# Kernel tuning notes

Measured on AMD Instinct MI355X. Metric: run time of the kernel, lower is better.

## Reference

```python
import jax, jax.numpy as jnp
import numpy as np

B, T, D, R = 8, 4096, 1024, 1024
INIT = 0.02

def setup_inputs() -> dict:
    key = jax.random.key(0)
    ks = jax.random.split(key, 8)
    x = jax.random.normal(ks[0], (B, T, D), dtype=jnp.float32)
    attention_mask = jnp.ones((B, T), dtype=bool)
    W_Q = jax.random.normal(ks[1], (D, D), dtype=jnp.float32) * (1.0 / np.sqrt(D))
    W_K = jax.random.normal(ks[2], (D, D), dtype=jnp.float32) * (1.0 / np.sqrt(D))
    U = jax.random.normal(ks[3], (D, R), dtype=jnp.float32) * INIT
    V = jax.random.normal(ks[4], (D, R), dtype=jnp.float32) * INIT
    Wb = jax.random.normal(ks[5], (D, R), dtype=jnp.float32) * INIT
    bias = jnp.zeros((D,), dtype=jnp.float32)
    W_O = jax.random.normal(ks[6], (D, D), dtype=jnp.float32) * (1.0 / np.sqrt(D))
    return {"x": x, "attention_mask": attention_mask, "W_Q": W_Q, "W_K": W_K,
            "U": U, "V": V, "Wb": Wb, "bias": bias, "W_O": W_O}

def reference(x, attention_mask, W_Q, W_K, U, V, Wb, bias, W_O):
    # Q = x @ W_Q^T, K = x @ W_K^T  (torch Linear stores weight as (out,in))
    Q = jnp.einsum('btd,ed->bte', x, W_Q)
    K = jnp.einsum('btd,ed->bte', x, W_K)
    m = attention_mask.astype(x.dtype)               # (B,T)
    A = Q @ V                                        # (B,T,R)  = Q_i V
    Kw = (K @ Wb) * m[..., None]                     # pad-masked K_j W
    S = jnp.cumsum(Kw, axis=1)                       # causal prefix sum over j<=i
    n = jnp.cumsum(m, axis=1)[..., None]             # n_valid per i, (B,T,1)
    # sum_{j<=i} BCN(Q_i,K_j) = ((Q_iV) * S_i) U^T + n_i * bias; then divide by max(n_i,1)
    out = ((A * S) @ U.T + n * bias) / jnp.clip(n, 1.0)
    return jnp.einsum('btd,ed->bte', out, W_O)
```

## Files before the change

kernel.cpp:

```cpp
#include <hip/hip_runtime.h>
#include <hip/hip_bf16.h>

typedef __attribute__((ext_vector_type(8))) short short8;
typedef __attribute__((ext_vector_type(4))) float f32x4;

#define Bc 8
#define Tc 4096
#define Dc 1024
#define Rc 1024
#define BT (Bc*Tc)

__device__ inline float b2f(ushort u) {
    union { float f; unsigned int i; } x; x.i = ((unsigned int)u) << 16; return x.f;
}
__device__ inline ushort f2b(float f) {
    union { float f; unsigned int i; } x; x.f = f;
    unsigned int r = x.i + 0x7fffu + ((x.i >> 16) & 1u);
    return (ushort)(r >> 16);
}

__device__ inline void gload16(const void* g, void* l) {
    __builtin_amdgcn_global_load_lds(
        (const __attribute__((address_space(1))) unsigned int*)g,
        (__attribute__((address_space(3))) unsigned int*)l, 16, 0, 0);
}


__device__ __attribute__((always_inline)) inline
short8 lds_frag(const char* mat, int rowbase, int k, int fr, int hi) {
    const int row = rowbase + fr;
    const int byte = (row << 7) + (((k << 6) + (hi << 4)) ^ ((row & 7) << 4));
    return *(const short8*)(mat + byte);
}

template<int KK>
__device__ __attribute__((always_inline)) inline
void rdb(const char* BB, short8 (&bf)[2][4], int wn, int fr, int hi) {
#pragma unroll
    for (int n = 0; n < 4; ++n)
        bf[KK][n] = lds_frag(BB, (wn << 6) + (n << 4), KK, fr, hi);
}

template<int MQ, int KK>
__device__ __attribute__((always_inline)) inline
void rda(const char* AB, short8 (&af)[4], int wm, int fr, int hi) {
#pragma unroll
    for (int i = 0; i < 4; ++i)
        af[i] = lds_frag(AB, (wm << 7) + ((MQ * 4 + i) << 4), KK, fr, hi);
}

template<int MQ, int KK>
__device__ __attribute__((always_inline)) inline
void mmq(f32x4 (&acc)[8][4], const short8 (&af)[4], const short8 (&bf)[2][4]) {
#pragma unroll
    for (int i = 0; i < 4; ++i)
#pragma unroll
        for (int n = 0; n < 4; ++n)
            acc[MQ * 4 + i][n] = __builtin_amdgcn_mfma_f32_16x16x32_bf16(
                af[i], bf[KK][n], acc[MQ * 4 + i][n], 0, 0, 0);
}

#define PH_MID do { __builtin_amdgcn_sched_barrier(0); __builtin_amdgcn_s_barrier(); \
    __builtin_amdgcn_s_setprio(1); } while (0)
#define PH_END do { __builtin_amdgcn_s_setprio(0); __builtin_amdgcn_sched_barrier(0); \
    __builtin_amdgcn_s_barrier(); } while (0)

#define STG(G, ld, thr, grow0, gk, lbase) do { \
    const ushort* _p = (G) + (size_t)(grow0) * (ld) + (gk); \
    gload16(_p + (thr), (lbase) + thrD); \
    gload16(_p + (size_t)64 * (ld) + (thr), (lbase) + thrD + 8192); } while (0)

#define TILE(cAb, cBb, stA, stB, tn, tn2) do { \
     \
    rdb<0>(cBb, bf, wn, fr, hi); \
    rda<0, 0>(cAb, afA, wm, fr, hi); \
    rda<1, 0>(cAb, afB, wm, fr, hi); \
    STG(A, lda, thrA, m0, (tn) << 6, stA); \
    PH_MID; mmq<0, 0>(acc, afA, bf); PH_END; \
     \
    rdb<1>(cBb, bf, wn, fr, hi); \
    rda<0, 1>(cAb, afA, wm, fr, hi); \
    STG(A, lda, thrA, m0 + 128, (tn) << 6, stA + 16384); \
    PH_MID; mmq<1, 0>(acc, afB, bf); PH_END; \
     \
    rda<1, 1>(cAb, afB, wm, fr, hi); \
    PH_MID; mmq<0, 1>(acc, afA, bf); PH_END; \
     \
    STG(Bt, ldb, thrB, n0,       (tn2) << 6, stB); \
    STG(Bt, ldb, thrB, n0 + 128, (tn2) << 6, stB + 16384); \
    PH_MID; mmq<1, 1>(acc, afB, bf); \
    __builtin_amdgcn_s_setprio(0); __builtin_amdgcn_sched_barrier(0); \
    asm volatile("s_waitcnt vmcnt(4)" ::: "memory"); \
    __builtin_amdgcn_s_barrier(); } while (0)

template<int EPI>
__global__ __launch_bounds__(512, 2)
void gemm256(const ushort* __restrict__ A, const ushort* __restrict__ Bt,
             void* __restrict__ Cout, const float* __restrict__ bias,
             int ntx, int K, int lda, int ldb, int ldc) {
    __shared__ __align__(16) char sA[65536];
    __shared__ __align__(16) char sB[65536];

    const int tid = threadIdx.x;
    const int w = tid >> 6, l = tid & 63;
    const int wm = w >> 2, wn = w & 3;
    const int fr = l & 15, hi = l >> 4;
    const int srow = (w << 3) + (l >> 3);
    const int scg = (((l & 7) ^ (l >> 3)) << 3);
    const size_t thrA = (size_t)srow * lda + scg;
    const size_t thrB = (size_t)srow * ldb + scg;
    const int thrD = (w << 10) + (l << 4);

    const int nwg = (int)gridDim.x;
    const int q = nwg >> 3;
    const int bid = (int)blockIdx.x;
    const int swz = (bid & 7) * q + (bid >> 3);
    const int by = swz / ntx, bx = swz % ntx;
    const int m0 = by << 8, n0 = bx << 8;

    f32x4 acc[8][4] = {};
    short8 afA[4], afB[4], bf[2][4];
    const int NT = K >> 6;

    STG(A,  lda, thrA, m0,        0,  sA);
    STG(A,  lda, thrA, m0 + 128,  0,  sA + 16384);
    STG(Bt, ldb, thrB, n0,        0,  sB);
    STG(Bt, ldb, thrB, n0 + 128,  0,  sB + 16384);
    STG(Bt, ldb, thrB, n0,        64, sB + 32768);
    STG(Bt, ldb, thrB, n0 + 128,  64, sB + 32768 + 16384);
    asm volatile("s_waitcnt vmcnt(4)" ::: "memory");
    __builtin_amdgcn_sched_barrier(0);
    __builtin_amdgcn_s_barrier();

    const char* cA0 = sA;
    const char* cB0 = sB;
    const char* cA1 = sA + 32768;
    const char* cB1 = sB + 32768;

    for (int it = 0; it < (NT >> 1); ++it) {
        const int t1 = 2 * it + 1;
        const int t2 = min(2 * it + 2, NT - 1);
        const int t3 = min(2 * it + 3, NT - 1);
        TILE(cA0, cB0, sA + 32768, sB, t1, t2);
        TILE(cA1, cB1, sA, sB + 32768, t2, t3);
    }

    const int crow = m0 + (wm << 7);
    const int ccol = n0 + (wn << 6);
#pragma unroll
    for (int m = 0; m < 8; ++m) {
#pragma unroll
        for (int n = 0; n < 4; ++n) {
            const int r0 = crow + (m << 4) + (hi << 2);
            const int c = ccol + (n << 4) + fr;
            if (EPI == 0) {
                ushort* C = (ushort*)Cout;
#pragma unroll
                for (int t = 0; t < 4; ++t)
                    C[(size_t)(r0 + t) * ldc + c] = f2b(acc[m][n][t]);
            } else {
                float* C = (float*)Cout;
                const float bv = bias[c];
#pragma unroll
                for (int t = 0; t < 4; ++t)
                    C[(size_t)(r0 + t) * ldc + c] = acc[m][n][t] + bv;
            }
        }
    }
}

__global__ void cast_f32_bf16(const float4* __restrict__ in, ushort4* __restrict__ out, int n4) {
    int i = blockIdx.x * blockDim.x + threadIdx.x;
    int stride = gridDim.x * blockDim.x;
    for (; i < n4; i += stride) {
        float4 v = in[i];
        ushort4 o;
        o.x = f2b(v.x); o.y = f2b(v.y); o.z = f2b(v.z); o.w = f2b(v.w);
        out[i] = o;
    }
}

__global__ void prep_weights(const float* __restrict__ V,  const float* __restrict__ Wb,
                             const float* __restrict__ U,  const float* __restrict__ WQ,
                             const float* __restrict__ WK, const float* __restrict__ WO,
                             ushort* __restrict__ Vt,  ushort* __restrict__ Wbt,
                             ushort* __restrict__ Ut,  ushort* __restrict__ WQt,
                             ushort* __restrict__ WKt, ushort* __restrict__ WOb) {
    __shared__ float tile[32][33];
    const float* in; ushort* out;
    switch (blockIdx.z) {
        case 0: in = V;  out = Vt;  break;
        case 1: in = Wb; out = Wbt; break;
        case 2: in = U;  out = Ut;  break;
        case 3: in = WQ; out = WQt; break;
        case 4: in = WK; out = WKt; break;
        default: in = WO; out = WOb; break;
    }
    int c0 = blockIdx.x * 32, r0 = blockIdx.y * 32;
    int tx = threadIdx.x & 31, ty = threadIdx.x >> 5;
    if (blockIdx.z < 5) {
        for (int i = 0; i < 32; i += 8)
            tile[ty + i][tx] = in[(size_t)(r0 + ty + i) * 1024 + c0 + tx];
        __syncthreads();
        for (int i = 0; i < 32; i += 8)
            out[(size_t)(c0 + ty + i) * 1024 + r0 + tx] = f2b(tile[tx][ty + i]);
    } else {
        for (int i = 0; i < 32; i += 8)
            out[(size_t)(r0 + ty + i) * 1024 + c0 + tx] =
                f2b(in[(size_t)(r0 + ty + i) * 1024 + c0 + tx]);
    }
}

__global__ __launch_bounds__(256)
void gemm_bt3(const ushort* __restrict__ Vt,  const ushort* __restrict__ WQt,
              const ushort* __restrict__ Wbt, const ushort* __restrict__ WKt,
              const ushort* __restrict__ WOb, const ushort* __restrict__ Ut,
              ushort* __restrict__ W1, ushort* __restrict__ Mmat) {
    const ushort *A, *Bt; ushort* Cout;
    switch (blockIdx.z) {
        case 0: A = Vt;  Bt = WQt; Cout = W1; break;
        case 1: A = Wbt; Bt = WKt; Cout = W1 + (size_t)Rc * Dc; break;
        default: A = WOb; Bt = Ut; Cout = Mmat; break;
    }
    __shared__ __align__(16) ushort As[128][32];
    __shared__ __align__(16) ushort Bs[128][32];
    const int tid = threadIdx.x;
    const int wave = tid >> 6, lane = tid & 63;
    const int m0 = blockIdx.y * 128, n0 = blockIdx.x * 128;
    const int wr = (wave >> 1) * 64, wc = (wave & 1) * 64;

    f32x4 acc[4][4] = {};

    const int rS = wave * 32 + (lane >> 2);
    const int kS = (lane & 3) * 8;
    const int fr = lane & 15;
    const int fq = (lane >> 4) * 8;

    for (int kt = 0; kt < 32; ++kt) {
        const int k0 = kt << 5;
        __syncthreads();
        gload16(A  + (size_t)(m0 + rS) * 1024      + k0 + kS, &As[rS][kS]);
        gload16(A  + (size_t)(m0 + rS + 16) * 1024 + k0 + kS, &As[rS + 16][kS]);
        gload16(Bt + (size_t)(n0 + rS) * 1024      + k0 + kS, &Bs[rS][kS]);
        gload16(Bt + (size_t)(n0 + rS + 16) * 1024 + k0 + kS, &Bs[rS + 16][kS]);
        __syncthreads();

        short8 af[4], bfr[4];
        #pragma unroll
        for (int i = 0; i < 4; i++) af[i]  = *(const short8*)&As[wr + i * 16 + fr][fq];
        #pragma unroll
        for (int i = 0; i < 4; i++) bfr[i] = *(const short8*)&Bs[wc + i * 16 + fr][fq];
        #pragma unroll
        for (int i = 0; i < 4; i++)
            #pragma unroll
            for (int j = 0; j < 4; j++)
                acc[i][j] = __builtin_amdgcn_mfma_f32_16x16x32_bf16(af[i], bfr[j], acc[i][j], 0, 0, 0);
    }

    const int rq = (lane >> 4) * 4;
    #pragma unroll
    for (int i = 0; i < 4; i++) {
        #pragma unroll
        for (int j = 0; j < 4; j++) {
            int row = m0 + wr + i * 16 + rq;
            int col = n0 + wc + j * 16 + fr;
            #pragma unroll
            for (int t = 0; t < 4; t++)
                Cout[(size_t)(row + t) * 1024 + col] = f2b(acc[i][j][t]);
        }
    }
}

__global__ void bias_O_kernel(const float* __restrict__ W_O, const float* __restrict__ bias,
                              float* __restrict__ biasO) {
    __shared__ float sh[256];
    int e = blockIdx.x, tid = threadIdx.x;
    float s = 0.f;
    for (int d = tid; d < Dc; d += 256) s += W_O[(size_t)e * Dc + d] * bias[d];
    sh[tid] = s; __syncthreads();
    for (int o = 128; o > 0; o >>= 1) { if (tid < o) sh[tid] += sh[tid + o]; __syncthreads(); }
    if (tid == 0) biasO[e] = sh[0];
}

__global__ void mask_scan(const int* __restrict__ mask, float* __restrict__ nbuf) {
    __shared__ float sh[256];
    int b = blockIdx.x, tid = threadIdx.x;
    float run = 0.f;
    for (int t0 = 0; t0 < Tc; t0 += 256) {
        float v = (mask[b * Tc + t0 + tid] != 0) ? 1.f : 0.f;
        sh[tid] = v; __syncthreads();
        for (int off = 1; off < 256; off <<= 1) {
            float add = (tid >= off) ? sh[tid - off] : 0.f;
            __syncthreads();
            sh[tid] += add;
            __syncthreads();
        }
        nbuf[b * Tc + t0 + tid] = run + sh[tid];
        run += sh[255];
        __syncthreads();
    }
}

#define NCHUNK 64
#define LCHUNK (Tc / NCHUNK)

__global__ void scan_partial(const ushort* __restrict__ AKw, const int* __restrict__ mask,
                             float* __restrict__ csum) {
    const int r = threadIdx.x * 4;
    const int chunk = blockIdx.x, b = blockIdx.y;
    const int row0 = b * Tc + chunk * LCHUNK;
    const ushort* p = AKw + (size_t)row0 * 2048 + 1024 + r;
    float4 s = {0.f, 0.f, 0.f, 0.f};
    for (int t = 0; t < LCHUNK; ++t) {
        if (mask[row0 + t] != 0) {
            ushort4 q = *(const ushort4*)(p + (size_t)t * 2048);
            s.x += b2f(q.x); s.y += b2f(q.y); s.z += b2f(q.z); s.w += b2f(q.w);
        }
    }
    *(float4*)(csum + (((size_t)b * NCHUNK + chunk) << 10) + r) = s;
}

__global__ void scan_offsets(float* __restrict__ csum) {
    const int r = threadIdx.x * 4;
    const int b = blockIdx.x;
    float4 run = {0.f, 0.f, 0.f, 0.f};
    for (int c = 0; c < NCHUNK; ++c) {
        float4* p = (float4*)(csum + (((size_t)b * NCHUNK + c) << 10) + r);
        float4 v = *p; *p = run;
        run.x += v.x; run.y += v.y; run.z += v.z; run.w += v.w;
    }
}

__global__ void scan_apply(ushort* __restrict__ AKw, const int* __restrict__ mask,
                           const float* __restrict__ csum, const float* __restrict__ nbuf) {
    const int r = threadIdx.x * 4;
    const int chunk = blockIdx.x, b = blockIdx.y;
    const int row0 = b * Tc + chunk * LCHUNK;
    float4 s = *(const float4*)(csum + (((size_t)b * NCHUNK + chunk) << 10) + r);
    ushort* p = AKw + (size_t)row0 * 2048 + r;
    for (int t = 0; t < LCHUNK; ++t) {
        const size_t off = (size_t)t * 2048;
        if (mask[row0 + t] != 0) {
            ushort4 kw = *(const ushort4*)(p + off + 1024);
            s.x += b2f(kw.x); s.y += b2f(kw.y); s.z += b2f(kw.z); s.w += b2f(kw.w);
        }
        const float rn = 1.f / fmaxf(nbuf[row0 + t], 1.f);
        ushort4 a = *(const ushort4*)(p + off);
        ushort4 o;
        o.x = f2b(b2f(a.x) * s.x * rn);
        o.y = f2b(b2f(a.y) * s.y * rn);
        o.z = f2b(b2f(a.z) * s.z * rn);
        o.w = f2b(b2f(a.w) * s.w * rn);
        *(ushort4*)(p + off) = o;
    }
}

extern "C" void kernel_launch(void* const* d_in, const int* in_sizes, int n_in,
                              void* d_out, int out_size, void* d_ws, size_t ws_size,
                              hipStream_t stream) {
    const float* x    = (const float*)d_in[0];
    const int*   mask = (const int*)d_in[1];
    const float* W_Q  = (const float*)d_in[2];
    const float* W_K  = (const float*)d_in[3];
    const float* U    = (const float*)d_in[4];
    const float* V    = (const float*)d_in[5];
    const float* Wb   = (const float*)d_in[6];
    const float* bias = (const float*)d_in[7];
    const float* W_O  = (const float*)d_in[8];
    float* out = (float*)d_out;

    char* ws = (char*)d_ws;
    ushort* xb   = (ushort*)ws; ws += (size_t)BT * Dc * 2;
    ushort* AKw  = (ushort*)ws; ws += (size_t)BT * 2048 * 2;
    ushort* W1   = (ushort*)ws; ws += (size_t)2048 * Dc * 2;
    ushort* Mmat = (ushort*)ws; ws += (size_t)Dc * Rc * 2;
    ushort* Vt   = (ushort*)ws; ws += (size_t)Dc * Rc * 2;
    ushort* Wbt  = (ushort*)ws; ws += (size_t)Dc * Rc * 2;
    ushort* Ut   = (ushort*)ws; ws += (size_t)Dc * Rc * 2;
    ushort* WQt  = (ushort*)ws; ws += (size_t)Dc * Dc * 2;
    ushort* WKt  = (ushort*)ws; ws += (size_t)Dc * Dc * 2;
    ushort* WOb  = (ushort*)ws; ws += (size_t)Dc * Dc * 2;
    float*  csum = (float*)ws;  ws += (size_t)Bc * NCHUNK * Rc * 4;
    float*  nbuf = (float*)ws;  ws += (size_t)Bc * Tc * 4;
    float*  biasO = (float*)ws; ws += (size_t)Dc * 4;

    cast_f32_bf16<<<2048, 256, 0, stream>>>((const float4*)x, (ushort4*)xb, BT * Dc / 4);
    prep_weights<<<dim3(32, 32, 6), 256, 0, stream>>>(V, Wb, U, W_Q, W_K, W_O,
                                                      Vt, Wbt, Ut, WQt, WKt, WOb);

    gemm_bt3<<<dim3(8, 8, 3), 256, 0, stream>>>(Vt, WQt, Wbt, WKt, WOb, Ut, W1, Mmat);
    bias_O_kernel<<<Dc, 256, 0, stream>>>(W_O, bias, biasO);

    gemm256<0><<<1024, 512, 0, stream>>>(xb, W1, AKw, nullptr, 8, Dc, Dc, Dc, 2048);

    mask_scan<<<Bc, 256, 0, stream>>>(mask, nbuf);
    scan_partial<<<dim3(NCHUNK, Bc), 256, 0, stream>>>(AKw, mask, csum);
    scan_offsets<<<Bc, 256, 0, stream>>>(csum);
    scan_apply<<<dim3(NCHUNK, Bc), 256, 0, stream>>>(AKw, mask, csum, nbuf);

    gemm256<1><<<512, 512, 0, stream>>>(AKw, Mmat, out, biasO, 4, Rc, 2048, Rc, Dc);
}
```

Baseline: 406.5 us.

## Fuse fp32-to-bf16 cast into first GEMM and compute chunk sums in epilogue

The first GEMM now reads fp32 x directly with register loads, converts to bf16 and writes to LDS itself, which removes the separate cast kernel and the bf16 copy of x. Its epilogue also computes the masked per-64-row chunk sums of the Kw half from fp32 accumulators, replacing the scan_partial kernel that re-read AKw. The cost is doubled global A traffic through registers instead of direct-to-LDS loads, which may disturb the carefully scheduled pipeline and add register pressure. The partial sums are now taken from fp32 accumulators rather than bf16-rounded values, so numerics change slightly.

```diff
diff --git a/kernel.cpp b/kernel.cpp
--- a/kernel.cpp
+++ b/kernel.cpp
@@ -18,6 +18,14 @@
     unsigned int r = x.i + 0x7fffu + ((x.i >> 16) & 1u);
     return (ushort)(r >> 16);
 }
+__device__ inline short8 pack8(float4 a, float4 b) {
+    short8 r;
+    r[0] = (short)f2b(a.x); r[1] = (short)f2b(a.y);
+    r[2] = (short)f2b(a.z); r[3] = (short)f2b(a.w);
+    r[4] = (short)f2b(b.x); r[5] = (short)f2b(b.y);
+    r[6] = (short)f2b(b.z); r[7] = (short)f2b(b.w);
+    return r;
+}
 
 __device__ inline void gload16(const void* g, void* l) {
     __builtin_amdgcn_global_load_lds(
@@ -70,36 +78,67 @@
     gload16(_p + (thr), (lbase) + thrD); \
     gload16(_p + (size_t)64 * (ld) + (thr), (lbase) + thrD + 8192); } while (0)
 
-#define TILE(cAb, cBb, stA, stB, tn, tn2) do { \
-     \
-    rdb<0>(cBb, bf, wn, fr, hi); \
-    rda<0, 0>(cAb, afA, wm, fr, hi); \
-    rda<1, 0>(cAb, afB, wm, fr, hi); \
-    STG(A, lda, thrA, m0, (tn) << 6, stA); \
-    PH_MID; mmq<0, 0>(acc, afA, bf); PH_END; \
-     \
-    rdb<1>(cBb, bf, wn, fr, hi); \
-    rda<0, 1>(cAb, afA, wm, fr, hi); \
-    STG(A, lda, thrA, m0 + 128, (tn) << 6, stA + 16384); \
-    PH_MID; mmq<1, 0>(acc, afB, bf); PH_END; \
-     \
-    rda<1, 1>(cAb, afB, wm, fr, hi); \
-    PH_MID; mmq<0, 1>(acc, afA, bf); PH_END; \
-     \
-    STG(Bt, ldb, thrB, n0,       (tn2) << 6, stB); \
-    STG(Bt, ldb, thrB, n0 + 128, (tn2) << 6, stB + 16384); \
-    PH_MID; mmq<1, 1>(acc, afB, bf); \
-    __builtin_amdgcn_s_setprio(0); __builtin_amdgcn_sched_barrier(0); \
-    asm volatile("s_waitcnt vmcnt(4)" ::: "memory"); \
-    __builtin_amdgcn_s_barrier(); } while (0)
-
-template<int EPI>
+#define TILEF(cAb, cBb, stA, stB, tn, tn2) do { \
+    { const float* _a = Af + (size_t)(m0 + srow) * lda + ((tn) << 6) + scg; \
+      float4 _v0 = *(const float4*)_a;              float4 _v1 = *(const float4*)(_a + 4); \
+      float4 _v2 = *(const float4*)(_a + 64 * lda); float4 _v3 = *(const float4*)(_a + 64 * lda + 4); \
+      rdb<0>(cBb, bf, wn, fr, hi); \
+      rda<0, 0>(cAb, afA, wm, fr, hi); \
+      rda<1, 0>(cAb, afB, wm, fr, hi); \
+      PH_MID; mmq<0, 0>(acc, afA, bf); \
+      *(short8*)((stA) + thrD) = pack8(_v0, _v1); \
+      *(short8*)((stA) + thrD + 8192) = pack8(_v2, _v3); \
+      PH_END; } \
+    { const float* _a = Af + (size_t)(m0 + 128 + srow) * lda + ((tn) << 6) + scg; \
+      float4 _v0 = *(const float4*)_a;              float4 _v1 = *(const float4*)(_a + 4); \
+      float4 _v2 = *(const float4*)(_a + 64 * lda); float4 _v3 = *(const float4*)(_a + 64 * lda + 4); \
+      rdb<1>(cBb, bf, wn, fr, hi); \
+      rda<0, 1>(cAb, afA, wm, fr, hi); \
+      PH_MID; mmq<1, 0>(acc, afB, bf); \
+      *(short8*)((stA) + 16384 + thrD) = pack8(_v0, _v1); \
+      *(short8*)((stA) + 16384 + thrD + 8192) = pack8(_v2, _v3); \
+      PH_END; } \
+    { rda<1, 1>(cAb, afB, wm, fr, hi); \
+      PH_MID; mmq<0, 1>(acc, afA, bf); PH_END; } \
+    { STG(Bt, ldb, thrB, n0,       (tn2) << 6, stB); \
+      STG(Bt, ldb, thrB, n0 + 128, (tn2) << 6, stB + 16384); \
+      PH_MID; mmq<1, 1>(acc, afB, bf); \
+      __builtin_amdgcn_s_setprio(0); __builtin_amdgcn_sched_barrier(0); \
+      asm volatile("s_waitcnt vmcnt(4)" ::: "memory"); \
+      __builtin_amdgcn_s_barrier(); } \
+} while (0)
+
+#define TILEB(cAb, cBb, stA, stB, tn, tn2) do { \
+    { rdb<0>(cBb, bf, wn, fr, hi); \
+      rda<0, 0>(cAb, afA, wm, fr, hi); \
+      rda<1, 0>(cAb, afB, wm, fr, hi); \
+      STG(Ab, lda, thrA, m0, (tn) << 6, stA); \
+      PH_MID; mmq<0, 0>(acc, afA, bf); PH_END; } \
+    { rdb<1>(cBb, bf, wn, fr, hi); \
+      rda<0, 1>(cAb, afA, wm, fr, hi); \
+      STG(Ab, lda, thrA, m0 + 128, (tn) << 6, stA + 16384); \
+      PH_MID; mmq<1, 0>(acc, afB, bf); PH_END; } \
+    { rda<1, 1>(cAb, afB, wm, fr, hi); \
+      PH_MID; mmq<0, 1>(acc, afA, bf); PH_END; } \
+    { STG(Bt, ldb, thrB, n0,       (tn2) << 6, stB); \
+      STG(Bt, ldb, thrB, n0 + 128, (tn2) << 6, stB + 16384); \
+      PH_MID; mmq<1, 1>(acc, afB, bf); \
+      __builtin_amdgcn_s_setprio(0); __builtin_amdgcn_sched_barrier(0); \
+      asm volatile("s_waitcnt vmcnt(4)" ::: "memory"); \
+      __builtin_amdgcn_s_barrier(); } \
+} while (0)
+
+template<int EPI, int AF32, int DOCS>
 __global__ __launch_bounds__(512, 2)
-void gemm256(const ushort* __restrict__ A, const ushort* __restrict__ Bt,
+void gemm256(const void* __restrict__ Ain, const ushort* __restrict__ Bt,
              void* __restrict__ Cout, const float* __restrict__ bias,
+             const float* __restrict__ maskf, float* __restrict__ csum,
              int ntx, int K, int lda, int ldb, int ldc) {
     __shared__ __align__(16) char sA[65536];
     __shared__ __align__(16) char sB[65536];
+
+    const float*  Af = (const float*)Ain;
+    const ushort* Ab = (const ushort*)Ain;
 
     const int tid = threadIdx.x;
     const int w = tid >> 6, l = tid & 63;
@@ -122,13 +161,31 @@
     short8 afA[4], afB[4], bf[2][4];
     const int NT = K >> 6;
 
-    STG(A,  lda, thrA, m0,        0,  sA);
-    STG(A,  lda, thrA, m0 + 128,  0,  sA + 16384);
-    STG(Bt, ldb, thrB, n0,        0,  sB);
-    STG(Bt, ldb, thrB, n0 + 128,  0,  sB + 16384);
-    STG(Bt, ldb, thrB, n0,        64, sB + 32768);
-    STG(Bt, ldb, thrB, n0 + 128,  64, sB + 32768 + 16384);
-    asm volatile("s_waitcnt vmcnt(4)" ::: "memory");
+    if (AF32) {
+        const float* _a = Af + (size_t)(m0 + srow) * lda + scg;
+        float4 v0 = *(const float4*)_a;              float4 v1 = *(const float4*)(_a + 4);
+        float4 v2 = *(const float4*)(_a + 64 * lda); float4 v3 = *(const float4*)(_a + 64 * lda + 4);
+        const float* _b = Af + (size_t)(m0 + 128 + srow) * lda + scg;
+        float4 u0 = *(const float4*)_b;              float4 u1 = *(const float4*)(_b + 4);
+        float4 u2 = *(const float4*)(_b + 64 * lda); float4 u3 = *(const float4*)(_b + 64 * lda + 4);
+        STG(Bt, ldb, thrB, n0,        0,  sB);
+        STG(Bt, ldb, thrB, n0 + 128,  0,  sB + 16384);
+        STG(Bt, ldb, thrB, n0,        64, sB + 32768);
+        STG(Bt, ldb, thrB, n0 + 128,  64, sB + 32768 + 16384);
+        *(short8*)(sA + thrD)                 = pack8(v0, v1);
+        *(short8*)(sA + thrD + 8192)          = pack8(v2, v3);
+        *(short8*)(sA + 16384 + thrD)         = pack8(u0, u1);
+        *(short8*)(sA + 16384 + thrD + 8192)  = pack8(u2, u3);
+        asm volatile("s_waitcnt vmcnt(4) lgkmcnt(0)" ::: "memory");
+    } else {
+        STG(Ab, lda, thrA, m0,        0,  sA);
+        STG(Ab, lda, thrA, m0 + 128,  0,  sA + 16384);
+        STG(Bt, ldb, thrB, n0,        0,  sB);
+        STG(Bt, ldb, thrB, n0 + 128,  0,  sB + 16384);
+        STG(Bt, ldb, thrB, n0,        64, sB + 32768);
+        STG(Bt, ldb, thrB, n0 + 128,  64, sB + 32768 + 16384);
+        asm volatile("s_waitcnt vmcnt(4)" ::: "memory");
+    }
     __builtin_amdgcn_sched_barrier(0);
     __builtin_amdgcn_s_barrier();
 
@@ -141,8 +198,13 @@
         const int t1 = 2 * it + 1;
         const int t2 = min(2 * it + 2, NT - 1);
         const int t3 = min(2 * it + 3, NT - 1);
-        TILE(cA0, cB0, sA + 32768, sB, t1, t2);
-        TILE(cA1, cB1, sA, sB + 32768, t2, t3);
+        if (AF32) {
+            TILEF(cA0, cB0, sA + 32768, sB, t1, t2);
+            TILEF(cA1, cB1, sA, sB + 32768, t2, t3);
+        } else {
+            TILEB(cA0, cB0, sA + 32768, sB, t1, t2);
+            TILEB(cA1, cB1, sA, sB + 32768, t2, t3);
+        }
     }
 
     const int crow = m0 + (wm << 7);
@@ -167,16 +229,34 @@
             }
         }
     }
-}
-
-__global__ void cast_f32_bf16(const float4* __restrict__ in, ushort4* __restrict__ out, int n4) {
-    int i = blockIdx.x * blockDim.x + threadIdx.x;
-    int stride = gridDim.x * blockDim.x;
-    for (; i < n4; i += stride) {
-        float4 v = in[i];
-        ushort4 o;
-        o.x = f2b(v.x); o.y = f2b(v.y); o.z = f2b(v.z); o.w = f2b(v.w);
-        out[i] = o;
+
+    if (DOCS && n0 >= 1024) {
+        const float* mrow = maskf + crow;
+#pragma unroll
+        for (int mh = 0; mh < 2; ++mh) {
+            float cs0 = 0.f, cs1 = 0.f, cs2 = 0.f, cs3 = 0.f;
+#pragma unroll
+            for (int mm = 0; mm < 4; ++mm) {
+                const int m = mh * 4 + mm;
+                const float4 mk = *(const float4*)(mrow + (m << 4) + (hi << 2));
+                cs0 += acc[m][0][0] * mk.x + acc[m][0][1] * mk.y + acc[m][0][2] * mk.z + acc[m][0][3] * mk.w;
+                cs1 += acc[m][1][0] * mk.x + acc[m][1][1] * mk.y + acc[m][1][2] * mk.z + acc[m][1][3] * mk.w;
+                cs2 += acc[m][2][0] * mk.x + acc[m][2][1] * mk.y + acc[m][2][2] * mk.z + acc[m][2][3] * mk.w;
+                cs3 += acc[m][3][0] * mk.x + acc[m][3][1] * mk.y + acc[m][3][2] * mk.z + acc[m][3][3] * mk.w;
+            }
+            float cs[4] = {cs0, cs1, cs2, cs3};
+            const int g = (crow + (mh << 6)) >> 6;
+#pragma unroll
+            for (int n = 0; n < 4; ++n) {
+                float v = cs[n];
+                v += __shfl_xor(v, 16, 64);
+                v += __shfl_xor(v, 32, 64);
+                if (hi == 0) {
+                    const int r = (ccol - 1024) + (n << 4) + fr;
+                    csum[(size_t)g * 1024 + r] = v;
+                }
+            }
+        }
     }
 }
 
@@ -282,12 +362,14 @@
     if (tid == 0) biasO[e] = sh[0];
 }
 
-__global__ void mask_scan(const int* __restrict__ mask, float* __restrict__ nbuf) {
+__global__ void mask_scan(const int* __restrict__ mask, float* __restrict__ nbuf,
+                          float* __restrict__ maskf) {
     __shared__ float sh[256];
     int b = blockIdx.x, tid = threadIdx.x;
     float run = 0.f;
     for (int t0 = 0; t0 < Tc; t0 += 256) {
         float v = (mask[b * Tc + t0 + tid] != 0) ? 1.f : 0.f;
+        maskf[b * Tc + t0 + tid] = v;
         sh[tid] = v; __syncthreads();
         for (int off = 1; off < 256; off <<= 1) {
             float add = (tid >= off) ? sh[tid - off] : 0.f;
@@ -303,22 +385,6 @@
 
 #define NCHUNK 64
 #define LCHUNK (Tc / NCHUNK)
-
-__global__ void scan_partial(const ushort* __restrict__ AKw, const int* __restrict__ mask,
-                             float* __restrict__ csum) {
-    const int r = threadIdx.x * 4;
-    const int chunk = blockIdx.x, b = blockIdx.y;
-    const int row0 = b * Tc + chunk * LCHUNK;
-    const ushort* p = AKw + (size_t)row0 * 2048 + 1024 + r;
-    float4 s = {0.f, 0.f, 0.f, 0.f};
-    for (int t = 0; t < LCHUNK; ++t) {
-        if (mask[row0 + t] != 0) {
-            ushort4 q = *(const ushort4*)(p + (size_t)t * 2048);
-            s.x += b2f(q.x); s.y += b2f(q.y); s.z += b2f(q.z); s.w += b2f(q.w);
-        }
-    }
-    *(float4*)(csum + (((size_t)b * NCHUNK + chunk) << 10) + r) = s;
-}
 
 __global__ void scan_offsets(float* __restrict__ csum) {
     const int r = threadIdx.x * 4;
@@ -370,7 +436,6 @@
     float* out = (float*)d_out;
 
     char* ws = (char*)d_ws;
-    ushort* xb   = (ushort*)ws; ws += (size_t)BT * Dc * 2;
     ushort* AKw  = (ushort*)ws; ws += (size_t)BT * 2048 * 2;
     ushort* W1   = (ushort*)ws; ws += (size_t)2048 * Dc * 2;
     ushort* Mmat = (ushort*)ws; ws += (size_t)Dc * Rc * 2;
@@ -382,21 +447,22 @@
     ushort* WOb  = (ushort*)ws; ws += (size_t)Dc * Dc * 2;
     float*  csum = (float*)ws;  ws += (size_t)Bc * NCHUNK * Rc * 4;
     float*  nbuf = (float*)ws;  ws += (size_t)Bc * Tc * 4;
+    float*  maskf= (float*)ws;  ws += (size_t)Bc * Tc * 4;
     float*  biasO = (float*)ws; ws += (size_t)Dc * 4;
 
-    cast_f32_bf16<<<2048, 256, 0, stream>>>((const float4*)x, (ushort4*)xb, BT * Dc / 4);
     prep_weights<<<dim3(32, 32, 6), 256, 0, stream>>>(V, Wb, U, W_Q, W_K, W_O,
                                                       Vt, Wbt, Ut, WQt, WKt, WOb);
+    mask_scan<<<Bc, 256, 0, stream>>>(mask, nbuf, maskf);
 
     gemm_bt3<<<dim3(8, 8, 3), 256, 0, stream>>>(Vt, WQt, Wbt, WKt, WOb, Ut, W1, Mmat);
     bias_O_kernel<<<Dc, 256, 0, stream>>>(W_O, bias, biasO);
 
-    gemm256<0><<<1024, 512, 0, stream>>>(xb, W1, AKw, nullptr, 8, Dc, Dc, Dc, 2048);
-
-    mask_scan<<<Bc, 256, 0, stream>>>(mask, nbuf);
-    scan_partial<<<dim3(NCHUNK, Bc), 256, 0, stream>>>(AKw, mask, csum);
+    gemm256<0, 1, 1><<<1024, 512, 0, stream>>>(x, W1, AKw, nullptr, maskf, csum,
+                                               8, Dc, Dc, Dc, 2048);
+
     scan_offsets<<<Bc, 256, 0, stream>>>(csum);
     scan_apply<<<dim3(NCHUNK, Bc), 256, 0, stream>>>(AKw, mask, csum, nbuf);
 
-    gemm256<1><<<512, 512, 0, stream>>>(AKw, Mmat, out, biasO, 4, Rc, 2048, Rc, Dc);
-}
+    gemm256<1, 0, 0><<<512, 512, 0, stream>>>(AKw, Mmat, out, biasO, nullptr, nullptr,
+                                              4, Rc, 2048, Rc, Dc);
+}
```

New measurement: 452.5 us. 1.11x slower.

## Fuse per-chunk Kw column sums into GEMM epilogue and drop scan kernels

Applied to the files above, without the earlier changes.

The first GEMM's epilogue now computes masked per-64-row column sums of the Kw half directly from fp32 accumulators and writes them to csum. This removes the scan_partial pass that re-read the Kw half of AKw, and the scan_offsets kernel, whose exclusive prefix is now summed per chunk inside scan_apply. The mask is pre-converted to floats earlier. The cost is extra epilogue work and shuffles in the GEMM, plus a redundant O(chunk) prefix loop in scan_apply. Sums also now come from unrounded fp32 accumulators rather than bf16 values.

```diff
diff --git a/kernel.cpp b/kernel.cpp
--- a/kernel.cpp
+++ b/kernel.cpp
@@ -75,12 +75,12 @@
     rdb<0>(cBb, bf, wn, fr, hi); \
     rda<0, 0>(cAb, afA, wm, fr, hi); \
     rda<1, 0>(cAb, afB, wm, fr, hi); \
-    STG(A, lda, thrA, m0, (tn) << 6, stA); \
+    STG(Ab, lda, thrA, m0, (tn) << 6, stA); \
     PH_MID; mmq<0, 0>(acc, afA, bf); PH_END; \
      \
     rdb<1>(cBb, bf, wn, fr, hi); \
     rda<0, 1>(cAb, afA, wm, fr, hi); \
-    STG(A, lda, thrA, m0 + 128, (tn) << 6, stA + 16384); \
+    STG(Ab, lda, thrA, m0 + 128, (tn) << 6, stA + 16384); \
     PH_MID; mmq<1, 0>(acc, afB, bf); PH_END; \
      \
     rda<1, 1>(cAb, afB, wm, fr, hi); \
@@ -93,10 +93,11 @@
     asm volatile("s_waitcnt vmcnt(4)" ::: "memory"); \
     __builtin_amdgcn_s_barrier(); } while (0)
 
-template<int EPI>
+template<int EPI, int DOCS>
 __global__ __launch_bounds__(512, 2)
-void gemm256(const ushort* __restrict__ A, const ushort* __restrict__ Bt,
+void gemm256(const ushort* __restrict__ Ab, const ushort* __restrict__ Bt,
              void* __restrict__ Cout, const float* __restrict__ bias,
+             const float* __restrict__ maskf, float* __restrict__ csum,
              int ntx, int K, int lda, int ldb, int ldc) {
     __shared__ __align__(16) char sA[65536];
     __shared__ __align__(16) char sB[65536];
@@ -122,8 +123,8 @@
     short8 afA[4], afB[4], bf[2][4];
     const int NT = K >> 6;
 
-    STG(A,  lda, thrA, m0,        0,  sA);
-    STG(A,  lda, thrA, m0 + 128,  0,  sA + 16384);
+    STG(Ab, lda, thrA, m0,        0,  sA);
+    STG(Ab, lda, thrA, m0 + 128,  0,  sA + 16384);
     STG(Bt, ldb, thrB, n0,        0,  sB);
     STG(Bt, ldb, thrB, n0 + 128,  0,  sB + 16384);
     STG(Bt, ldb, thrB, n0,        64, sB + 32768);
@@ -164,6 +165,35 @@
 #pragma unroll
                 for (int t = 0; t < 4; ++t)
                     C[(size_t)(r0 + t) * ldc + c] = acc[m][n][t] + bv;
+            }
+        }
+    }
+
+    if (DOCS && n0 >= 1024) {
+        const float* mrow = maskf + crow;
+#pragma unroll
+        for (int mh = 0; mh < 2; ++mh) {
+            float cs0 = 0.f, cs1 = 0.f, cs2 = 0.f, cs3 = 0.f;
+#pragma unroll
+            for (int mm = 0; mm < 4; ++mm) {
+                const int m = mh * 4 + mm;
+                const float4 mk = *(const float4*)(mrow + (m << 4) + (hi << 2));
+                cs0 += acc[m][0][0] * mk.x + acc[m][0][1] * mk.y + acc[m][0][2] * mk.z + acc[m][0][3] * mk.w;
+                cs1 += acc[m][1][0] * mk.x + acc[m][1][1] * mk.y + acc[m][1][2] * mk.z + acc[m][1][3] * mk.w;
+                cs2 += acc[m][2][0] * mk.x + acc[m][2][1] * mk.y + acc[m][2][2] * mk.z + acc[m][2][3] * mk.w;
+                cs3 += acc[m][3][0] * mk.x + acc[m][3][1] * mk.y + acc[m][3][2] * mk.z + acc[m][3][3] * mk.w;
+            }
+            float cs[4] = {cs0, cs1, cs2, cs3};
+            const int g = (crow + (mh << 6)) >> 6;
+#pragma unroll
+            for (int n = 0; n < 4; ++n) {
+                float v = cs[n];
+                v += __shfl_xor(v, 16, 64);
+                v += __shfl_xor(v, 32, 64);
+                if (hi == 0) {
+                    const int r = (ccol - 1024) + (n << 4) + fr;
+                    csum[(size_t)g * 1024 + r] = v;
+                }
             }
         }
     }
@@ -282,12 +312,14 @@
     if (tid == 0) biasO[e] = sh[0];
 }
 
-__global__ void mask_scan(const int* __restrict__ mask, float* __restrict__ nbuf) {
+__global__ void mask_scan(const int* __restrict__ mask, float* __restrict__ nbuf,
+                          float* __restrict__ maskf) {
     __shared__ float sh[256];
     int b = blockIdx.x, tid = threadIdx.x;
     float run = 0.f;
     for (int t0 = 0; t0 < Tc; t0 += 256) {
         float v = (mask[b * Tc + t0 + tid] != 0) ? 1.f : 0.f;
+        maskf[b * Tc + t0 + tid] = v;
         sh[tid] = v; __syncthreads();
         for (int off = 1; off < 256; off <<= 1) {
             float add = (tid >= off) ? sh[tid - off] : 0.f;
@@ -304,39 +336,16 @@
 #define NCHUNK 64
 #define LCHUNK (Tc / NCHUNK)
 
-__global__ void scan_partial(const ushort* __restrict__ AKw, const int* __restrict__ mask,
-                             float* __restrict__ csum) {
-    const int r = threadIdx.x * 4;
-    const int chunk = blockIdx.x, b = blockIdx.y;
-    const int row0 = b * Tc + chunk * LCHUNK;
-    const ushort* p = AKw + (size_t)row0 * 2048 + 1024 + r;
-    float4 s = {0.f, 0.f, 0.f, 0.f};
-    for (int t = 0; t < LCHUNK; ++t) {
-        if (mask[row0 + t] != 0) {
-            ushort4 q = *(const ushort4*)(p + (size_t)t * 2048);
-            s.x += b2f(q.x); s.y += b2f(q.y); s.z += b2f(q.z); s.w += b2f(q.w);
-        }
-    }
-    *(float4*)(csum + (((size_t)b * NCHUNK + chunk) << 10) + r) = s;
-}
-
-__global__ void scan_offsets(float* __restrict__ csum) {
-    const int r = threadIdx.x * 4;
-    const int b = blockIdx.x;
-    float4 run = {0.f, 0.f, 0.f, 0.f};
-    for (int c = 0; c < NCHUNK; ++c) {
-        float4* p = (float4*)(csum + (((size_t)b * NCHUNK + c) << 10) + r);
-        float4 v = *p; *p = run;
-        run.x += v.x; run.y += v.y; run.z += v.z; run.w += v.w;
-    }
-}
-
 __global__ void scan_apply(ushort* __restrict__ AKw, const int* __restrict__ mask,
                            const float* __restrict__ csum, const float* __restrict__ nbuf) {
     const int r = threadIdx.x * 4;
     const int chunk = blockIdx.x, b = blockIdx.y;
     const int row0 = b * Tc + chunk * LCHUNK;
-    float4 s = *(const float4*)(csum + (((size_t)b * NCHUNK + chunk) << 10) + r);
+    float4 s = {0.f, 0.f, 0.f, 0.f};
+    for (int c = 0; c < chunk; ++c) {
+        float4 v = *(const float4*)(csum + (((size_t)b * NCHUNK + c) << 10) + r);
+        s.x += v.x; s.y += v.y; s.z += v.z; s.w += v.w;
+    }
     ushort* p = AKw + (size_t)row0 * 2048 + r;
     for (int t = 0; t < LCHUNK; ++t) {
         const size_t off = (size_t)t * 2048;
@@ -382,21 +391,22 @@
     ushort* WOb  = (ushort*)ws; ws += (size_t)Dc * Dc * 2;
     float*  csum = (float*)ws;  ws += (size_t)Bc * NCHUNK * Rc * 4;
     float*  nbuf = (float*)ws;  ws += (size_t)Bc * Tc * 4;
+    float*  maskf= (float*)ws;  ws += (size_t)Bc * Tc * 4;
     float*  biasO = (float*)ws; ws += (size_t)Dc * 4;
 
     cast_f32_bf16<<<2048, 256, 0, stream>>>((const float4*)x, (ushort4*)xb, BT * Dc / 4);
     prep_weights<<<dim3(32, 32, 6), 256, 0, stream>>>(V, Wb, U, W_Q, W_K, W_O,
                                                       Vt, Wbt, Ut, WQt, WKt, WOb);
+    mask_scan<<<Bc, 256, 0, stream>>>(mask, nbuf, maskf);
 
     gemm_bt3<<<dim3(8, 8, 3), 256, 0, stream>>>(Vt, WQt, Wbt, WKt, WOb, Ut, W1, Mmat);
     bias_O_kernel<<<Dc, 256, 0, stream>>>(W_O, bias, biasO);
 
-    gemm256<0><<<1024, 512, 0, stream>>>(xb, W1, AKw, nullptr, 8, Dc, Dc, Dc, 2048);
-
-    mask_scan<<<Bc, 256, 0, stream>>>(mask, nbuf);
-    scan_partial<<<dim3(NCHUNK, Bc), 256, 0, stream>>>(AKw, mask, csum);
-    scan_offsets<<<Bc, 256, 0, stream>>>(csum);
+    gemm256<0, 1><<<1024, 512, 0, stream>>>(xb, W1, AKw, nullptr, maskf, csum,
+                                            8, Dc, Dc, Dc, 2048);
+
     scan_apply<<<dim3(NCHUNK, Bc), 256, 0, stream>>>(AKw, mask, csum, nbuf);
 
-    gemm256<1><<<512, 512, 0, stream>>>(AKw, Mmat, out, biasO, 4, Rc, 2048, Rc, Dc);
-}
+    gemm256<1, 0><<<512, 512, 0, stream>>>(AKw, Mmat, out, biasO, nullptr, nullptr,
+                                           4, Rc, 2048, Rc, Dc);
+}
```

Measured after the change: 394.0 us. 1.03x faster.
